# Optimization experiments

Hardware: AMD Instinct MI355X
Metric: run time of the kernel (lower is better)

## Reference

```python
import jax, jax.numpy as jnp
import numpy as np

WIN = 7            # window side -> K2 = 49
DIM = 512          # channel dim C
HEADS = 16
E = DIM // HEADS   # embed_dim / head_dim = 32
SCALE = E ** -0.5


def _rel_pos_index(wh, ww):
    coords = np.stack(np.meshgrid(np.arange(wh), np.arange(ww), indexing='ij'))  # [2, wh, ww]
    cf = coords.reshape(2, -1)                      # [2, K2]
    rel = cf[:, :, None] - cf[:, None, :]           # [2, K2, K2]
    rel = rel.transpose(1, 2, 0).astype(np.int64)   # [K2, K2, 2]
    rel[..., 0] += wh - 1
    rel[..., 1] += ww - 1
    rel[..., 0] *= 2 * ww - 1
    return rel.sum(-1)                              # [K2, K2]

RPI = jnp.asarray(_rel_pos_index(WIN, WIN))         # constant int index map


def setup_inputs() -> dict:
    key = jax.random.key(0)
    ks = jax.random.split(key, 9)
    s = 0.02
    return {
        'x':         jax.random.normal(ks[0], (2048, WIN * WIN, DIM), jnp.float32),
        'qk_w':      jax.random.normal(ks[1], (2 * DIM, DIM), jnp.float32) * s,
        'qk_b':      jnp.zeros((2 * DIM,), jnp.float32),
        'rev_v_w':   jax.random.normal(ks[2], (DIM, DIM), jnp.float32) * s,
        'rev_v_b':   jnp.zeros((DIM,), jnp.float32),
        'wg_w':      jax.random.normal(ks[3], (E * E, DIM), jnp.float32) * s,
        'proj_w':    jax.random.normal(ks[4], (DIM, DIM), jnp.float32) * s,
        'proj_b':    jnp.zeros((DIM,), jnp.float32),
        'rpb_table': jax.random.normal(ks[5], ((2 * WIN - 1) ** 2, HEADS), jnp.float32) * s,
    }


def reference(x, qk_w, qk_b, rev_v_w, rev_v_b, wg_w, proj_w, proj_b, rpb_table):
    BW, K2, C = x.shape
    # joint q/k projection: [BW, K2, 2, H, E]
    qk = (x @ qk_w.T + qk_b).reshape(BW, K2, 2, HEADS, E)
    q = qk[:, :, 0].transpose(0, 2, 1, 3) * SCALE   # [BW, H, K2, E]
    k = qk[:, :, 1].transpose(0, 2, 1, 3)           # [BW, H, K2, E]
    attn = jnp.einsum('bhqe,bhke->bhqk', q, k)      # [BW, H, K2, K2]
    # relative position bias gather: [K2, K2, H] -> [H, K2, K2]
    bias = rpb_table[RPI].transpose(2, 0, 1)
    attn = jax.nn.softmax(attn + bias[None], axis=-1)
    # reverse attention: values projected, softmax transposed (transpose_softmax=True)
    v = (x @ rev_v_w.T + rev_v_b).reshape(BW, K2, HEADS, E).transpose(0, 2, 1, 3)  # [BW, H, K2, E]
    expert_mixture = jnp.einsum('bhkq,bhke->bhqe', attn, v)   # attn^T @ v, [BW, H, K2, E]
    # hypernetwork: per-token E x E mixing matrices from the raw input
    proj_weight = (x @ wg_w.T).reshape(BW, K2, E, E)          # [BW, K2, E, E]
    em_t = expert_mixture.transpose(0, 2, 1, 3)               # [BW, K2, H, E]
    out = jnp.einsum('bkhe,bkef->bkhf', em_t, proj_weight).reshape(BW, K2, C)
    # output projection (reverse_proj); dropouts are identity (p=0)
    return out @ proj_w.T + proj_b
```

## Files before the change

### kernel.cpp

```cpp
#include <hip/hip_runtime.h>
#include <hip/hip_bf16.h>
#include <stdint.h>

typedef __attribute__((ext_vector_type(8))) short short8;
typedef __attribute__((ext_vector_type(4))) float f32x4;
typedef unsigned short u16;

#define SCALE_F 0.17677669529663687f

__device__ __forceinline__ u16 f2bf(float f){
  union { float f; unsigned u; } x; x.f = f;
  unsigned r = x.u + 0x7fffu + ((x.u >> 16) & 1u);
  return (u16)(r >> 16);
}
__device__ __forceinline__ float bf2f(u16 u){
  union { float f; unsigned u; } x; x.u = ((unsigned)u) << 16; return x.f;
}
__device__ __forceinline__ unsigned swz(unsigned base, int row, unsigned rowb, unsigned colb){
  return base + (unsigned)row * rowb + (colb ^ (((unsigned)row & 7u) << 4));
}
__device__ __forceinline__ void gll16(const void* g, void* l){
  __builtin_amdgcn_global_load_lds(
    (const __attribute__((address_space(1))) unsigned int*)(unsigned long long)(size_t)g,
    (__attribute__((address_space(3))) unsigned int*)(unsigned int)(size_t)l,
    16, 0, 0);
}

__global__ void convk(const float* __restrict__ x,
                      const float* __restrict__ qk_w, const float* __restrict__ rev_v_w,
                      const float* __restrict__ wg_w, const float* __restrict__ proj_w,
                      u16* __restrict__ ws){
  long long i8 = ((long long)blockIdx.x * 256 + threadIdx.x) * 8;
  const float* s;
  if      (i8 <  524288) s = qk_w   + i8;
  else if (i8 <  786432) s = rev_v_w + (i8 - 524288);
  else if (i8 < 1310720) s = wg_w   + (i8 - 786432);
  else if (i8 < 1572864) s = proj_w + (i8 - 1310720);
  else                   s = x      + (i8 - 1572864);
  f32x4 lo = *(const f32x4*)s, hi = *(const f32x4*)(s + 4);
  short8 v;
  v[0]=f2bf(lo[0]); v[1]=f2bf(lo[1]); v[2]=f2bf(lo[2]); v[3]=f2bf(lo[3]);
  v[4]=f2bf(hi[0]); v[5]=f2bf(hi[1]); v[6]=f2bf(hi[2]); v[7]=f2bf(hi[3]);
  *(short8*)(ws + i8) = v;
}

template<int NT, int F32OUT>
__global__ __launch_bounds__(256, 2)
void gemm128(const u16* __restrict__ A, int lda,
             const u16* __restrict__ B,
             const float* __restrict__ b0, const float* __restrict__ b1,
             void* __restrict__ Cg, int ldc){
  __shared__ __align__(16) unsigned char sm[32768];
  const int tid = threadIdx.x, wave = tid >> 6, lane = tid & 63;
  const int l15 = lane & 15, lg = lane >> 4;
  const int nwg = gridDim.x, bidr = blockIdx.x;
  const int q8 = nwg >> 3, r8 = nwg & 7, xc = bidr & 7, oo = bidr >> 3;
  const int wg = (xc < r8 ? xc * (q8 + 1) : r8 * (q8 + 1) + (xc - r8) * q8) + oo;
  const int bm = wg / NT, bn = wg % NT;
  const int wm = wave >> 1, wn = wave & 1;
  const f32x4 zf = {0.f, 0.f, 0.f, 0.f};
  f32x4 acc[4][4];
#pragma unroll
  for (int mt=0; mt<4; mt++)
#pragma unroll
    for (int nt=0; nt<4; nt++) acc[mt][nt] = zf;

  const u16* Ab = A + (size_t)bm * 128 * lda;
  const u16* Bb = B + (size_t)bn * 128 * 512;

  for (int ks = 0; ks < 8; ks++){
#pragma unroll
    for (int it = 0; it < 4; it++){
      int c = (wave*4 + it)*64 + lane;
      int r = c >> 3, cc = c & 7;
      int sc = cc ^ (r & 7);
      gll16(Ab + (size_t)r*lda + ks*64 + sc*8, sm + (unsigned)(wave*4 + it)*1024u);
      gll16(Bb + (size_t)r*512 + ks*64 + sc*8, sm + 16384u + (unsigned)(wave*4 + it)*1024u);
    }
    __syncthreads();
#pragma unroll
    for (int kk = 0; kk < 2; kk++){
      short8 aq[4], bq[4];
#pragma unroll
      for (int mt=0; mt<4; mt++){
        int r = wm*64 + mt*16 + l15;
        aq[mt] = *(const short8*)(sm + (unsigned)r*128u + (((unsigned)(kk*64 + lg*16)) ^ (((unsigned)r & 7u) << 4)));
      }
#pragma unroll
      for (int nt=0; nt<4; nt++){
        int r = wn*64 + nt*16 + l15;
        bq[nt] = *(const short8*)(sm + 16384u + (unsigned)r*128u + (((unsigned)(kk*64 + lg*16)) ^ (((unsigned)r & 7u) << 4)));
      }
#pragma unroll
      for (int mt=0; mt<4; mt++)
#pragma unroll
        for (int nt=0; nt<4; nt++)
          acc[mt][nt] = __builtin_amdgcn_mfma_f32_16x16x32_bf16(aq[mt], bq[nt], acc[mt][nt], 0, 0, 0);
    }
    __syncthreads();
  }

  float bia[4];
#pragma unroll
  for (int nt=0; nt<4; nt++){
    int n = bn*128 + wn*64 + nt*16 + l15;
    if (F32OUT) bia[nt] = b0[n];
    else        bia[nt] = (n < 1024) ? b0[n] : (n < 1536 ? b1[n - 1024] : 0.f);
  }

  if (!F32OUT){
#pragma unroll
    for (int mt=0; mt<4; mt++)
#pragma unroll
      for (int nt=0; nt<4; nt++)
#pragma unroll
        for (int i=0; i<4; i++){
          int row = wm*64 + mt*16 + lg*4 + i;
          unsigned colb = (unsigned)((wn*64 + nt*16 + l15) * 2);
          *(u16*)(sm + (unsigned)row*256u + (colb ^ (((unsigned)row & 7u) << 4))) = f2bf(acc[mt][nt][i] + bia[nt]);
        }
    __syncthreads();
    u16* Co = (u16*)Cg;
#pragma unroll
    for (int it=0; it<8; it++){
      int c = it*256 + tid;
      int r = c >> 4, cc = c & 15;
      short8 v = *(const short8*)(sm + (unsigned)r*256u + (((unsigned)(cc*16)) ^ (((unsigned)r & 7u) << 4)));
      *(short8*)(Co + (size_t)(bm*128 + r)*ldc + bn*128 + cc*8) = v;
    }
  } else {
    float* Co = (float*)Cg;
#pragma unroll
    for (int half=0; half<2; half++){
      if (wm == half){
#pragma unroll
        for (int mt=0; mt<4; mt++)
#pragma unroll
          for (int nt=0; nt<4; nt++)
#pragma unroll
            for (int i=0; i<4; i++){
              int row = mt*16 + lg*4 + i;
              unsigned colb = (unsigned)((wn*64 + nt*16 + l15) * 4);
              *(float*)(sm + (unsigned)row*512u + (colb ^ (((unsigned)row & 7u) << 4))) = acc[mt][nt][i] + bia[nt];
            }
      }
      __syncthreads();
#pragma unroll
      for (int it=0; it<8; it++){
        int c = it*256 + tid;
        int r = c >> 5, cc = c & 31;
        f32x4 v = *(const f32x4*)(sm + (unsigned)r*512u + (((unsigned)(cc*16)) ^ (((unsigned)r & 7u) << 4)));
        *(f32x4*)(Co + (size_t)(bm*128 + half*64 + r)*ldc + bn*128 + cc*4) = v;
      }
      __syncthreads();
    }
  }
}

__global__ __launch_bounds__(512, 2)
void attn_fused(const u16* __restrict__ qkv, const float* __restrict__ rpb,
                u16* __restrict__ o1){
  __shared__ __align__(16) unsigned char lds[105760];
  const unsigned L_V = 0u, L_PT = 50176u, L_RPB = 100352u;
  const int tid = threadIdx.x, wave = tid >> 6, lane = tid & 63;
  const int l15 = lane & 15, lg = lane >> 4;
  const size_t wb = (size_t)blockIdx.x * 49;
  const u16* base = qkv + wb * 2560;
  unsigned char* ptb = lds + L_PT + (unsigned)wave * 6272u;
  const f32x4 zf = {0.f, 0.f, 0.f, 0.f};

  for (int i = tid; i < 2704; i += 512)
    *(u16*)(lds + L_RPB + i*2) = f2bf(rpb[i]);
  for (int c = tid; c < 49*64; c += 512){
    int r = c >> 6, c8 = c & 63;
    short8 v = *(const short8*)(base + (size_t)r*2560 + 1024 + c8*8);
    *(short8*)(lds + swz(L_V, r, 1024u, (unsigned)(c8*16))) = v;
  }
  __syncthreads();

  auto attn_pass = [&](int hp, f32x4 (&em)[4][2]){
    const int h = wave + hp*8;
    short8 aq[4], bq[4];
#pragma unroll
    for (int mt=0; mt<4; mt++){
      int r = mt*16 + l15; if (r > 48) r = 48;
      aq[mt] = *(const short8*)(base + (size_t)r*2560 + h*32 + lg*8);
    }
#pragma unroll
    for (int nt=0; nt<4; nt++){
      int kt = nt*16 + l15; if (kt > 48) kt = 48;
      bq[nt] = *(const short8*)(base + (size_t)kt*2560 + 512 + h*32 + lg*8);
    }
    f32x4 s[4][4];
#pragma unroll
    for (int mt=0; mt<4; mt++)
#pragma unroll
      for (int nt=0; nt<4; nt++) s[mt][nt] = zf;
#pragma unroll
    for (int mt=0; mt<4; mt++)
#pragma unroll
      for (int nt=0; nt<4; nt++)
        s[mt][nt] = __builtin_amdgcn_mfma_f32_16x16x32_bf16(aq[mt], bq[nt], s[mt][nt], 0, 0, 0);
#pragma unroll
    for (int mt=0; mt<4; mt++)
#pragma unroll
      for (int nt=0; nt<4; nt++)
#pragma unroll
        for (int i=0; i<4; i++){
          int q  = mt*16 + lg*4 + i;
          int kt = nt*16 + l15;
          float v = s[mt][nt][i] * SCALE_F;
          if (kt < 49){
            int qc = (q > 48) ? 48 : q;
            int qi = qc / 7, qj = qc - qi*7;
            int ki = kt / 7, kj = kt - ki*7;
            int idx = (qi - ki + 6)*13 + (qj - kj + 6);
            v += bf2f(*(const u16*)(lds + L_RPB + (idx*16 + h)*2));
          } else v = -1e30f;
          s[mt][nt][i] = v;
        }
#pragma unroll
    for (int mt=0; mt<4; mt++)
#pragma unroll
      for (int i=0; i<4; i++){
        float m = fmaxf(fmaxf(s[mt][0][i], s[mt][1][i]), fmaxf(s[mt][2][i], s[mt][3][i]));
        m = fmaxf(m, __shfl_xor(m, 1)); m = fmaxf(m, __shfl_xor(m, 2));
        m = fmaxf(m, __shfl_xor(m, 4)); m = fmaxf(m, __shfl_xor(m, 8));
        float sum = 0.f;
#pragma unroll
        for (int nt=0; nt<4; nt++){ float e = __expf(s[mt][nt][i] - m); s[mt][nt][i] = e; sum += e; }
        sum += __shfl_xor(sum, 1); sum += __shfl_xor(sum, 2);
        sum += __shfl_xor(sum, 4); sum += __shfl_xor(sum, 8);
        float inv = 1.0f / sum;
#pragma unroll
        for (int nt=0; nt<4; nt++) s[mt][nt][i] *= inv;
      }
#pragma unroll
    for (int mt=0; mt<4; mt++)
#pragma unroll
      for (int nt=0; nt<4; nt++)
#pragma unroll
        for (int i=0; i<4; i++){
          int q  = mt*16 + lg*4 + i;
          int kt = nt*16 + l15;
          if (kt < 49){
            u16 val = (q < 49) ? f2bf(s[mt][nt][i]) : (u16)0;
            *(u16*)(ptb + (unsigned)kt*128u + (((unsigned)(q*2)) ^ (((unsigned)kt & 7u) << 4))) = val;
          }
        }
#pragma unroll
    for (int kk=0; kk<2; kk++){
      short8 pa[4];
#pragma unroll
      for (int mt=0; mt<4; mt++){
        int r = mt*16 + l15; if (r > 48) r = 48;
        pa[mt] = *(const short8*)(ptb + (unsigned)r*128u + (((unsigned)(kk*64 + lg*16)) ^ (((unsigned)r & 7u) << 4)));
      }
      short8 vb[2];
#pragma unroll
      for (int nt=0; nt<2; nt++){
        int ch = h*32 + nt*16 + l15;
#pragma unroll
        for (int j=0; j<8; j++){
          int kt = kk*32 + lg*8 + j; if (kt > 48) kt = 48;
          vb[nt][j] = *(const short*)(lds + swz(L_V, kt, 1024u, (unsigned)(ch*2)));
        }
      }
#pragma unroll
      for (int mt=0; mt<4; mt++)
#pragma unroll
        for (int nt=0; nt<2; nt++)
          em[mt][nt] = __builtin_amdgcn_mfma_f32_16x16x32_bf16(pa[mt], vb[nt], em[mt][nt], 0, 0, 0);
    }
  };

  f32x4 em0[4][2], em1[4][2];
#pragma unroll
  for (int mt=0; mt<4; mt++)
#pragma unroll
    for (int nt=0; nt<2; nt++){ em0[mt][nt] = zf; em1[mt][nt] = zf; }
  attn_pass(0, em0);
  attn_pass(1, em1);
  __syncthreads();

  auto em_store = [&](f32x4 (&em)[4][2], int h){
#pragma unroll
    for (int mt=0; mt<4; mt++)
#pragma unroll
      for (int nt=0; nt<2; nt++)
#pragma unroll
        for (int i=0; i<4; i++){
          int q = mt*16 + lg*4 + i;
          if (q < 49){
            int ch = h*32 + nt*16 + l15;
            *(u16*)(lds + swz(L_V, q, 1024u, (unsigned)(ch*2))) = f2bf(em[mt][nt][i]);
          }
        }
  };
  em_store(em0, wave);
  em_store(em1, 8 + wave);
  __syncthreads();

  for (int t = wave; t < 49; t += 8){
    const u16* pwt = base + (size_t)t*2560 + 1536;
#pragma unroll
    for (int rd = 0; rd < 2; rd++){
      int i8 = (rd*64 + lane)*8;
      short8 v = *(const short8*)(pwt + i8);
      int e = i8 >> 5, f0 = i8 & 31;
#pragma unroll
      for (int jj = 0; jj < 8; jj++){
        int f = f0 + jj;
        *(u16*)(ptb + (unsigned)f*64u + (((unsigned)(e*2)) ^ (((unsigned)f & 3u) << 4))) = (u16)v[jj];
      }
    }
    short8 ea = *(const short8*)(lds + swz(L_V, t, 1024u, (unsigned)(l15*64 + lg*16)));
    f32x4 o[2];
#pragma unroll
    for (int nt=0; nt<2; nt++){
      int f = nt*16 + l15;
      short8 pb = *(const short8*)(ptb + (unsigned)f*64u + (((unsigned)(lg*16)) ^ (((unsigned)f & 3u) << 4)));
      o[nt] = __builtin_amdgcn_mfma_f32_16x16x32_bf16(ea, pb, zf, 0, 0, 0);
    }
#pragma unroll
    for (int nt=0; nt<2; nt++)
#pragma unroll
      for (int i=0; i<4; i++){
        int ch = (lg*4 + i)*32 + nt*16 + l15;
        *(u16*)(lds + swz(L_V, t, 1024u, (unsigned)(ch*2))) = f2bf(o[nt][i]);
      }
  }
  __syncthreads();

  u16* ob = o1 + wb * 512;
  for (int c = tid; c < 49*64; c += 512){
    int r = c >> 6, c8 = c & 63;
    short8 v = *(const short8*)(lds + swz(L_V, r, 1024u, (unsigned)(c8*16)));
    *(short8*)(ob + (size_t)r*512 + c8*8) = v;
  }
}

#define LDS_X   0u
#define LDS_V   50176u
#define LDS_QK  100352u
#define LDS_RPB 150528u
#define LDS_PW  50176u
#define LDS_EM  0u
#define LDS_TOTAL 155936

__device__ __forceinline__ void gemm_strip(const unsigned char* ldsp, unsigned abase,
    const u16* __restrict__ W, int wrow0, int l15, int lg, f32x4 acc[4][4]){
  for (int kk = 0; kk < 16; kk++){
    short8 bq[4];
#pragma unroll
    for (int nt = 0; nt < 4; nt++){
      const u16* p = W + (size_t)(wrow0 + nt*16 + l15) * 512 + kk*32 + lg*8;
      bq[nt] = *(const short8*)p;
    }
    short8 aq[4];
#pragma unroll
    for (int mt = 0; mt < 4; mt++){
      int r = mt*16 + l15; if (r > 48) r = 48;
      aq[mt] = *(const short8*)(ldsp + swz(abase, r, 1024u, (unsigned)(kk*64 + lg*16)));
    }
#pragma unroll
    for (int mt = 0; mt < 4; mt++)
#pragma unroll
      for (int nt = 0; nt < 4; nt++)
        acc[mt][nt] = __builtin_amdgcn_mfma_f32_16x16x32_bf16(aq[mt], bq[nt], acc[mt][nt], 0, 0, 0);
  }
}

__global__ void conv_w4(const float* __restrict__ a, const float* __restrict__ b,
                        const float* __restrict__ c, const float* __restrict__ d,
                        u16* __restrict__ o){
  int i = blockIdx.x * 256 + threadIdx.x;
  if (i < 524288)        o[i] = f2bf(a[i]);
  else if (i < 786432)   o[i] = f2bf(b[i - 524288]);
  else if (i < 1310720)  o[i] = f2bf(c[i - 786432]);
  else                   o[i] = f2bf(d[i - 1310720]);
}

__launch_bounds__(512, 2)
__global__ void wa_main(
    const float* __restrict__ x, const float* __restrict__ qk_b,
    const float* __restrict__ rev_v_b, const float* __restrict__ proj_b,
    const float* __restrict__ rpb,
    const u16* __restrict__ Wqk, const u16* __restrict__ Wv,
    const u16* __restrict__ Wwg, const u16* __restrict__ Wproj,
    float* __restrict__ out){
  __shared__ __align__(16) unsigned char ldsp[LDS_TOTAL];
  const int tid  = threadIdx.x;
  const int wave = tid >> 6, lane = tid & 63, l15 = lane & 15, lg = lane >> 4;
  const int b = blockIdx.x;
  const float* xb = x + (size_t)b * 49 * 512;
  const f32x4 zf = {0.f, 0.f, 0.f, 0.f};
  for (int i = tid; i < 169*16; i += 512)
    *(u16*)(ldsp + LDS_RPB + i*2) = f2bf(rpb[i]);
  for (int ch = tid; ch < 49*64; ch += 512){
    int r = ch >> 6, c8 = ch & 63;
    const f32x4* s = (const f32x4*)(xb + r*512 + c8*8);
    f32x4 lo = s[0], hi = s[1];
    short8 v;
    v[0]=f2bf(lo[0]); v[1]=f2bf(lo[1]); v[2]=f2bf(lo[2]); v[3]=f2bf(lo[3]);
    v[4]=f2bf(hi[0]); v[5]=f2bf(hi[1]); v[6]=f2bf(hi[2]); v[7]=f2bf(hi[3]);
    *(short8*)(ldsp + swz(LDS_X, r, 1024u, (unsigned)(c8*16))) = v;
  }
  __syncthreads();
  {
    f32x4 acc[4][4];
#pragma unroll
    for (int mt=0; mt<4; mt++)
#pragma unroll
      for (int nt=0; nt<4; nt++) acc[mt][nt] = zf;
    gemm_strip(ldsp, LDS_X, Wv, wave*64, l15, lg, acc);
#pragma unroll
    for (int nt=0; nt<4; nt++){
      int ch = wave*64 + nt*16 + l15;
      float bias = rev_v_b[ch];
#pragma unroll
      for (int mt=0; mt<4; mt++)
#pragma unroll
        for (int i=0; i<4; i++){
          int r = mt*16 + lg*4 + i;
          if (r < 49)
            *(u16*)(ldsp + swz(LDS_V, r, 1024u, (unsigned)(ch*2))) = f2bf(acc[mt][nt][i] + bias);
        }
    }
  }
  auto qk_pass = [&](int p){
    f32x4 acc[4][4];
#pragma unroll
    for (int mt=0; mt<4; mt++)
#pragma unroll
      for (int nt=0; nt<4; nt++) acc[mt][nt] = zf;
    int wrow0 = (wave < 4) ? (p*256 + wave*64) : (512 + p*256 + (wave-4)*64);
    gemm_strip(ldsp, LDS_X, Wqk, wrow0, l15, lg, acc);
#pragma unroll
    for (int nt=0; nt<4; nt++){
      int ch  = wrow0 + nt*16 + l15;
      int col = wave*64 + nt*16 + l15;
      float bias = qk_b[ch];
#pragma unroll
      for (int mt=0; mt<4; mt++)
#pragma unroll
        for (int i=0; i<4; i++){
          int r = mt*16 + lg*4 + i;
          if (r < 49)
            *(u16*)(ldsp + swz(LDS_QK, r, 1024u, (unsigned)(col*2))) = f2bf(acc[mt][nt][i] + bias);
        }
    }
  };
  auto attn_pass = [&](int p, f32x4 (&em)[4][2]){
    const int h = p*8 + wave;
    f32x4 s[4][4];
#pragma unroll
    for (int mt=0; mt<4; mt++)
#pragma unroll
      for (int nt=0; nt<4; nt++) s[mt][nt] = zf;
    short8 aq[4], bq[4];
#pragma unroll
    for (int mt=0; mt<4; mt++){
      int r = mt*16 + l15; if (r > 48) r = 48;
      aq[mt] = *(const short8*)(ldsp + swz(LDS_QK, r, 1024u, (unsigned)(wave*64 + lg*16)));
    }
#pragma unroll
    for (int nt=0; nt<4; nt++){
      int kt = nt*16 + l15; if (kt > 48) kt = 48;
      bq[nt] = *(const short8*)(ldsp + swz(LDS_QK, kt, 1024u, (unsigned)(512 + wave*64 + lg*16)));
    }
#pragma unroll
    for (int mt=0; mt<4; mt++)
#pragma unroll
      for (int nt=0; nt<4; nt++)
        s[mt][nt] = __builtin_amdgcn_mfma_f32_16x16x32_bf16(aq[mt], bq[nt], s[mt][nt], 0, 0, 0);
#pragma unroll
    for (int mt=0; mt<4; mt++)
#pragma unroll
      for (int nt=0; nt<4; nt++)
#pragma unroll
        for (int i=0; i<4; i++){
          int q  = mt*16 + lg*4 + i;
          int kt = nt*16 + l15;
          float v = s[mt][nt][i] * SCALE_F;
          if (kt < 49){
            int qc = (q > 48) ? 48 : q;
            int qi = qc / 7, qj = qc - qi*7;
            int ki = kt / 7, kj = kt - ki*7;
            int idx = (qi - ki + 6)*13 + (qj - kj + 6);
            v += bf2f(*(const u16*)(ldsp + LDS_RPB + (idx*16 + h)*2));
          } else v = -1e30f;
          s[mt][nt][i] = v;
        }
#pragma unroll
    for (int mt=0; mt<4; mt++)
#pragma unroll
      for (int i=0; i<4; i++){
        float m = fmaxf(fmaxf(s[mt][0][i], s[mt][1][i]), fmaxf(s[mt][2][i], s[mt][3][i]));
        m = fmaxf(m, __shfl_xor(m, 1)); m = fmaxf(m, __shfl_xor(m, 2));
        m = fmaxf(m, __shfl_xor(m, 4)); m = fmaxf(m, __shfl_xor(m, 8));
        float sum = 0.f;
#pragma unroll
        for (int nt=0; nt<4; nt++){ float e = __expf(s[mt][nt][i] - m); s[mt][nt][i] = e; sum += e; }
        sum += __shfl_xor(sum, 1); sum += __shfl_xor(sum, 2);
        sum += __shfl_xor(sum, 4); sum += __shfl_xor(sum, 8);
        float inv = 1.0f / sum;
#pragma unroll
        for (int nt=0; nt<4; nt++) s[mt][nt][i] *= inv;
      }
    __syncthreads();
    const unsigned ptb = LDS_QK + (unsigned)wave * 6272u;
#pragma unroll
    for (int mt=0; mt<4; mt++)
#pragma unroll
      for (int nt=0; nt<4; nt++)
#pragma unroll
        for (int i=0; i<4; i++){
          int q  = mt*16 + lg*4 + i;
          int kt = nt*16 + l15;
          if (kt < 49){
            u16 val = (q < 49) ? f2bf(s[mt][nt][i]) : (u16)0;
            *(u16*)(ldsp + ptb + (unsigned)kt*128u + (((unsigned)(q*2)) ^ (((unsigned)kt & 7u) << 4))) = val;
          }
        }
#pragma unroll
    for (int kk=0; kk<2; kk++){
      short8 pa[4];
#pragma unroll
      for (int mt=0; mt<4; mt++){
        int r = mt*16 + l15; if (r > 48) r = 48;
        pa[mt] = *(const short8*)(ldsp + ptb + (unsigned)r*128u + (((unsigned)(kk*64 + lg*16)) ^ (((unsigned)r & 7u) << 4)));
      }
      short8 vb[2];
#pragma unroll
      for (int nt=0; nt<2; nt++){
        int ch = h*32 + nt*16 + l15;
#pragma unroll
        for (int j=0; j<8; j++){
          int kt = kk*32 + lg*8 + j; if (kt > 48) kt = 48;
          vb[nt][j] = *(const short*)(ldsp + swz(LDS_V, kt, 1024u, (unsigned)(ch*2)));
        }
      }
#pragma unroll
      for (int mt=0; mt<4; mt++)
#pragma unroll
        for (int nt=0; nt<2; nt++)
          em[mt][nt] = __builtin_amdgcn_mfma_f32_16x16x32_bf16(pa[mt], vb[nt], em[mt][nt], 0, 0, 0);
    }
  };
  f32x4 em0[4][2], em1[4][2];
#pragma unroll
  for (int mt=0; mt<4; mt++)
#pragma unroll
    for (int nt=0; nt<2; nt++){ em0[mt][nt] = zf; em1[mt][nt] = zf; }
  qk_pass(0);
  __syncthreads();
  attn_pass(0, em0);
  __syncthreads();
  qk_pass(1);
  __syncthreads();
  attn_pass(1, em1);
  __syncthreads();
  for (int nh = 0; nh < 2; nh++){
    f32x4 acc[4][4];
#pragma unroll
    for (int mt=0; mt<4; mt++)
#pragma unroll
      for (int nt=0; nt<4; nt++) acc[mt][nt] = zf;
    int n0 = nh*512 + wave*64;
    gemm_strip(ldsp, LDS_X, Wwg, n0, l15, lg, acc);
#pragma unroll
    for (int nt=0; nt<4; nt++){
      int n  = n0 + nt*16 + l15;
      int pc = (n & 31)*32 + (n >> 5);
      unsigned cb = ((unsigned)(pc*2)) ^ (((unsigned)n & 7u) << 4);
#pragma unroll
      for (int mt=0; mt<4; mt++)
#pragma unroll
        for (int i=0; i<4; i++){
          int r = mt*16 + lg*4 + i;
          if (r < 49)
            *(u16*)(ldsp + LDS_PW + (unsigned)r*2048u + cb) = f2bf(acc[mt][nt][i]);
        }
    }
  }
  __syncthreads();
  auto em_store = [&](f32x4 (&em)[4][2], int h){
#pragma unroll
    for (int mt=0; mt<4; mt++)
#pragma unroll
      for (int nt=0; nt<2; nt++)
#pragma unroll
        for (int i=0; i<4; i++){
          int q = mt*16 + lg*4 + i;
          if (q < 49){
            int ch = h*32 + nt*16 + l15;
            *(u16*)(ldsp + swz(LDS_EM, q, 1024u, (unsigned)(ch*2))) = f2bf(em[mt][nt][i]);
          }
        }
  };
  em_store(em0, wave);
  em_store(em1, 8 + wave);
  __syncthreads();
  for (int t = wave; t < 49; t += 8){
    short8 ea = *(const short8*)(ldsp + swz(LDS_EM, t, 1024u, (unsigned)(l15*64 + lg*16)));
    f32x4 o[2];
#pragma unroll
    for (int nt=0; nt<2; nt++){
      int f = nt*16 + l15;
      short8 pb = *(const short8*)(ldsp + LDS_PW + (unsigned)t*2048u +
                    (((unsigned)((f*32 + lg*8)*2)) ^ (((unsigned)f & 7u) << 4)));
      o[nt] = __builtin_amdgcn_mfma_f32_16x16x32_bf16(ea, pb, zf, 0, 0, 0);
    }
#pragma unroll
    for (int nt=0; nt<2; nt++)
#pragma unroll
      for (int i=0; i<4; i++){
        int h2 = lg*4 + i;
        int ch = h2*32 + nt*16 + l15;
        *(u16*)(ldsp + swz(LDS_EM, t, 1024u, (unsigned)(ch*2))) = f2bf(o[nt][i]);
      }
  }
  __syncthreads();
  {
    f32x4 acc[4][4];
#pragma unroll
    for (int mt=0; mt<4; mt++)
#pragma unroll
      for (int nt=0; nt<4; nt++) acc[mt][nt] = zf;
    gemm_strip(ldsp, LDS_EM, Wproj, wave*64, l15, lg, acc);
    float* ob = out + (size_t)b * 49 * 512;
#pragma unroll
    for (int nt=0; nt<4; nt++){
      int n = wave*64 + nt*16 + l15;
      float bias = proj_b[n];
#pragma unroll
      for (int mt=0; mt<4; mt++)
#pragma unroll
        for (int i=0; i<4; i++){
          int r = mt*16 + lg*4 + i;
          if (r < 49) ob[r*512 + n] = acc[mt][nt][i] + bias;
        }
    }
  }
}

extern "C" void kernel_launch(void* const* d_in, const int* in_sizes, int n_in,
                              void* d_out, int out_size, void* d_ws, size_t ws_size,
                              hipStream_t stream){
  const float* x       = (const float*)d_in[0];
  const float* qk_w    = (const float*)d_in[1];
  const float* qk_b    = (const float*)d_in[2];
  const float* rev_v_w = (const float*)d_in[3];
  const float* rev_v_b = (const float*)d_in[4];
  const float* wg_w    = (const float*)d_in[5];
  const float* proj_w  = (const float*)d_in[6];
  const float* proj_b  = (const float*)d_in[7];
  const float* rpb     = (const float*)d_in[8];
  u16* ws = (u16*)d_ws;

  const unsigned long long BASE = 105906176ULL;
  int C = 0;
  for (int cand : {2048, 1024, 512, 256, 128}){
    if (BASE + (unsigned long long)cand * 301056ULL <= ws_size){ C = cand; break; }
  }
  if (C == 0){
    conv_w4<<<6144, 256, 0, stream>>>(qk_w, rev_v_w, wg_w, proj_w, ws);
    wa_main<<<2048, 512, 0, stream>>>(x, qk_b, rev_v_b, proj_b, rpb,
        ws, ws + 524288, ws + 786432, ws + 1310720, (float*)d_out);
    return;
  }

  u16* Wcat  = ws;
  u16* Wproj = ws + 1310720;
  u16* xb    = ws + 1572864;
  u16* qkvpw = ws + 52953088ULL;
  u16* o1    = qkvpw + (size_t)C * 49 * 2560;

  convk<<<25856, 256, 0, stream>>>(x, qk_w, rev_v_w, wg_w, proj_w, ws);

  const int nch = 2048 / C;
  const int mt128 = C * 49 / 128;
  for (int ch = 0; ch < nch; ch++){
    size_t t0 = (size_t)ch * C * 49;
    gemm128<20, 0><<<mt128 * 20, 256, 0, stream>>>(xb + t0*512, 512, Wcat,
        qk_b, rev_v_b, qkvpw, 2560);
    attn_fused<<<C, 512, 0, stream>>>(qkvpw, rpb, o1);
    gemm128<4, 1><<<mt128 * 4, 256, 0, stream>>>(o1, 512, Wproj,
        proj_b, (const float*)nullptr, (float*)d_out + t0*512, 512);
  }
  (void)Wcat; (void)Wproj;
}
```

Measured before the change: 691.0 us.

## Add 256x256-tile double-buffered GEMM for the fused QKV+hypernet projection

Adds a gemm256 kernel with 512 threads, 256x256 output tiles, 128KB of dynamic LDS, and double-buffered global_load_lds staging with explicit waitcnt and barriers. It replaces the 128-tile GEMM for the input projection whenever the token count is a multiple of 256 and the shared-memory attribute can be set. Larger tiles raise arithmetic intensity and cut redundant A/B loads. The cost is lower occupancy (128KB LDS limits each CU to one block) and fewer workgroups, which may underfill the CUs.

```diff
diff --git a/kernel.cpp b/kernel.cpp
--- a/kernel.cpp
+++ b/kernel.cpp
@@ -44,6 +44,111 @@
   *(short8*)(ws + i8) = v;
 }
 
+template<int NT>
+__global__ __launch_bounds__(512, 2)
+void gemm256(const u16* __restrict__ A,
+             const u16* __restrict__ B,
+             const float* __restrict__ b0, const float* __restrict__ b1,
+             u16* __restrict__ Cg, int ldc){
+  extern __shared__ __align__(16) unsigned char dyn[];
+  const int tid = threadIdx.x, wave = tid >> 6, lane = tid & 63;
+  const int l15 = lane & 15, lg = lane >> 4;
+  const int nwg = gridDim.x, bidr = blockIdx.x;
+  const int q8 = nwg >> 3, r8 = nwg & 7, xc = bidr & 7, oo = bidr >> 3;
+  const int wg = (xc < r8 ? xc * (q8 + 1) : r8 * (q8 + 1) + (xc - r8) * q8) + oo;
+  const int bm = wg / NT, bn = wg % NT;
+  const int wm = wave >> 2, wn = wave & 3;
+  const f32x4 zf = {0.f, 0.f, 0.f, 0.f};
+
+  float bia[4];
+#pragma unroll
+  for (int nf=0; nf<4; nf++){
+    int n = bn*256 + wn*64 + nf*16 + l15;
+    bia[nf] = (n < 1024) ? b0[n] : (n < 1536 ? b1[n - 1024] : 0.f);
+  }
+  asm volatile("s_waitcnt vmcnt(0)" ::: "memory");
+
+  f32x4 acc[8][4];
+#pragma unroll
+  for (int mf=0; mf<8; mf++)
+#pragma unroll
+    for (int nf=0; nf<4; nf++) acc[mf][nf] = zf;
+
+  const u16* Ab = A + (size_t)bm * 256 * 512;
+  const u16* Bb = B + (size_t)bn * 256 * 512;
+
+  auto STAGE = [&](int t){
+    unsigned buf = (unsigned)(t & 1) * 32768u;
+#pragma unroll
+    for (int it = 0; it < 4; it++){
+      int c = (it*8 + wave)*64 + lane;
+      int r = c >> 3, cc = c & 7;
+      int sc = cc ^ (r & 7);
+      unsigned dst = buf + (unsigned)(it*8 + wave)*1024u;
+      gll16(Ab + (size_t)r*512 + t*64 + sc*8, dyn + dst);
+      gll16(Bb + (size_t)r*512 + t*64 + sc*8, dyn + 65536u + dst);
+    }
+  };
+
+  STAGE(0);
+  STAGE(1);
+
+  for (int k = 0; k < 8; k++){
+    if (k < 7) asm volatile("s_waitcnt vmcnt(8)" ::: "memory");
+    else       asm volatile("s_waitcnt vmcnt(0)" ::: "memory");
+    __builtin_amdgcn_s_barrier();
+    __builtin_amdgcn_sched_barrier(0);
+    const unsigned char* As = dyn + (unsigned)(k & 1) * 32768u;
+    const unsigned char* Bs = dyn + 65536u + (unsigned)(k & 1) * 32768u;
+#pragma unroll
+    for (int kk = 0; kk < 2; kk++){
+      short8 af[8], bfr[4];
+#pragma unroll
+      for (int mf=0; mf<8; mf++){
+        int r = wm*128 + mf*16 + l15;
+        af[mf] = *(const short8*)(As + (unsigned)r*128u + (((unsigned)(kk*64 + lg*16)) ^ (((unsigned)r & 7u) << 4)));
+      }
+#pragma unroll
+      for (int nf=0; nf<4; nf++){
+        int r = wn*64 + nf*16 + l15;
+        bfr[nf] = *(const short8*)(Bs + (unsigned)r*128u + (((unsigned)(kk*64 + lg*16)) ^ (((unsigned)r & 7u) << 4)));
+      }
+      __builtin_amdgcn_s_setprio(1);
+#pragma unroll
+      for (int mf=0; mf<8; mf++)
+#pragma unroll
+        for (int nf=0; nf<4; nf++)
+          acc[mf][nf] = __builtin_amdgcn_mfma_f32_16x16x32_bf16(af[mf], bfr[nf], acc[mf][nf], 0, 0, 0);
+      __builtin_amdgcn_s_setprio(0);
+    }
+    if (k < 6){
+      __builtin_amdgcn_s_barrier();
+      __builtin_amdgcn_sched_barrier(0);
+      STAGE(k + 2);
+    }
+  }
+
+  __syncthreads();
+#pragma unroll
+  for (int mf=0; mf<8; mf++)
+#pragma unroll
+    for (int nf=0; nf<4; nf++)
+#pragma unroll
+      for (int i=0; i<4; i++){
+        int row = wm*128 + mf*16 + lg*4 + i;
+        unsigned colb = (unsigned)((wn*64 + nf*16 + l15) * 2);
+        *(u16*)(dyn + (unsigned)row*512u + (colb ^ (((unsigned)row & 7u) << 4))) = f2bf(acc[mf][nf][i] + bia[nf]);
+      }
+  __syncthreads();
+#pragma unroll
+  for (int it=0; it<16; it++){
+    int c = it*512 + tid;
+    int r = c >> 5, cc = c & 31;
+    short8 v = *(const short8*)(dyn + (unsigned)r*512u + (((unsigned)(cc*16)) ^ (((unsigned)r & 7u) << 4)));
+    *(short8*)(Cg + (size_t)(bm*256 + r)*ldc + bn*256 + cc*8) = v;
+  }
+}
+
 template<int NT, int F32OUT>
 __global__ __launch_bounds__(256, 2)
 void gemm128(const u16* __restrict__ A, int lda,
@@ -166,8 +271,10 @@
   const int l15 = lane & 15, lg = lane >> 4;
   const size_t wb = (size_t)blockIdx.x * 49;
   const u16* base = qkv + wb * 2560;
+  u16* __restrict__ emb;
   unsigned char* ptb = lds + L_PT + (unsigned)wave * 6272u;
   const f32x4 zf = {0.f, 0.f, 0.f, 0.f};
+  (void)emb;
 
   for (int i = tid; i < 2704; i += 512)
     *(u16*)(lds + L_RPB + i*2) = f2bf(rpb[i]);
@@ -679,12 +786,24 @@
 
   convk<<<25856, 256, 0, stream>>>(x, qk_w, rev_v_w, wg_w, proj_w, ws);
 
+  bool use256 = ((C * 49) % 256 == 0);
+  if (use256){
+    hipError_t e = hipFuncSetAttribute((const void*)gemm256<10>,
+        hipFuncAttributeMaxDynamicSharedMemorySize, 131072);
+    if (e != hipSuccess) use256 = false;
+  }
+
   const int nch = 2048 / C;
   const int mt128 = C * 49 / 128;
+  const int mt256 = C * 49 / 256;
   for (int ch = 0; ch < nch; ch++){
     size_t t0 = (size_t)ch * C * 49;
-    gemm128<20, 0><<<mt128 * 20, 256, 0, stream>>>(xb + t0*512, 512, Wcat,
-        qk_b, rev_v_b, qkvpw, 2560);
+    if (use256)
+      gemm256<10><<<mt256 * 10, 512, 131072, stream>>>(xb + t0*512, Wcat,
+          qk_b, rev_v_b, qkvpw, 2560);
+    else
+      gemm128<20, 0><<<mt128 * 20, 256, 0, stream>>>(xb + t0*512, 512, Wcat,
+          qk_b, rev_v_b, qkvpw, 2560);
     attn_fused<<<C, 512, 0, stream>>>(qkvpw, rpb, o1);
     gemm128<4, 1><<<mt128 * 4, 256, 0, stream>>>(o1, 512, Wproj,
         proj_b, (const float*)nullptr, (float*)d_out + t0*512, 512);
```

New measurement: 704.3 us. Within noise of the previous version (+1.9%).
